# Kernel tuning notes

Hardware: AMD Instinct MI355X
Metric: run time of the kernel (lower is better)

The kernel has to match this reference:

```python
import math
import jax, jax.numpy as jnp
import numpy as np

B = 128          # batch_size (graphs)
SEQ = 128        # max_seq_len (nodes per graph)
D = 128          # input_dim
HID = 64         # enc_hidden_dim
HEADS = 4        # in_head
N = B * SEQ      # total nodes
E = 262144       # edges (avg degree 16)


def _make_pe(seq, d):
    pos = np.arange(seq, dtype=np.float32)[:, None]
    i_even = np.arange(0, d, 2, dtype=np.float32)
    pe = np.zeros((seq, d), dtype=np.float32)
    pe[:, 0::2] = np.sin(pos / 10000.0 ** (2.0 * i_even / d))
    pe[:, 1::2] = np.cos(pos / 10000.0 ** (2.0 * (i_even + 1.0) / d))
    return jnp.asarray(pe)


def setup_inputs() -> dict:
    key = jax.random.key(0)
    ks = jax.random.split(key, 10)
    s = 0.1
    return {
        "x": jax.random.normal(ks[0], (N, D), jnp.float32),
        "edge_index": jax.random.randint(ks[1], (2, E), 0, N),
        "pe": _make_pe(SEQ, D),
        "W1": jax.random.normal(ks[2], (D, HEADS * HID), jnp.float32) * s,
        "a_src1": jax.random.normal(ks[3], (HEADS, HID), jnp.float32) * s,
        "a_dst1": jax.random.normal(ks[4], (HEADS, HID), jnp.float32) * s,
        "b1": jnp.zeros((HEADS * HID,), jnp.float32),
        "W2": jax.random.normal(ks[5], (HEADS * HID, HID), jnp.float32) * s,
        "a_src2": jax.random.normal(ks[6], (1, HID), jnp.float32) * s,
        "a_dst2": jax.random.normal(ks[7], (1, HID), jnp.float32) * s,
        "b2": jnp.zeros((HID,), jnp.float32),
        "batch_size": B,
    }


def _gat_conv(x, src, dst, W, a_src, a_dst, b, heads, ch, concat, n):
    # PyG GATConv (eval mode, self-loops already appended to src/dst).
    h = (x @ W).reshape(n, heads, ch)                      # [N,H,C]
    alpha_src = jnp.einsum("nhc,hc->nh", h, a_src)         # [N,H]
    alpha_dst = jnp.einsum("nhc,hc->nh", h, a_dst)
    e = jax.nn.leaky_relu(alpha_src[src] + alpha_dst[dst], 0.2)  # [E,H]
    m = jax.ops.segment_max(e, dst, num_segments=n)        # segment softmax over dst
    ex = jnp.exp(e - m[dst])
    den = jax.ops.segment_sum(ex, dst, num_segments=n)
    alpha = ex / (den[dst] + 1e-16)                        # [E,H]
    out = jax.ops.segment_sum(h[src] * alpha[:, :, None], dst, num_segments=n)
    out = out.reshape(n, heads * ch) if concat else out.mean(axis=1)
    return out + b


def reference(x, edge_index, pe, W1, a_src1, a_dst1, b1, W2, a_src2, a_dst2, b2, batch_size):
    n = x.shape[0]
    loop = jnp.arange(n)
    src = jnp.concatenate([edge_index[0], loop])           # add self-loops (PyG default)
    dst = jnp.concatenate([edge_index[1], loop])
    # positional encoding (dropout inactive in eval)
    h = x * math.sqrt(x.shape[1]) + jnp.tile(pe, (batch_size, 1))
    h = jax.nn.elu(_gat_conv(h, src, dst, W1, a_src1, a_dst1, b1, HEADS, HID, True, n))
    out = _gat_conv(h, src, dst, W2, a_src2, a_dst2, b2, 1, HID, False, n)
    return out.reshape(batch_size, -1, out.shape[1])
```

## Files before the change

### kernel.cpp

```cpp
#include <hip/hip_runtime.h>
#include <hip/hip_bf16.h>

typedef __hip_bfloat16 bf16;
typedef __attribute__((ext_vector_type(8))) short short8v;
typedef __attribute__((ext_vector_type(4))) float f32x4;

#define N_NODES 16384
#define D_IN    128
#define HID     64
#define HEADS   4
#define F1      256
#define SEQ     128
#define SLOTS   64

__device__ __forceinline__ float wave_sum(float v) {
    #pragma unroll
    for (int o = 32; o > 0; o >>= 1) v += __shfl_xor(v, o, 64);
    return v;
}
__device__ __forceinline__ float lrelu(float v) { return v > 0.f ? v : 0.2f * v; }
__device__ __forceinline__ float bfu(unsigned short u) {
    return __uint_as_float((unsigned)u << 16);
}
__device__ __forceinline__ unsigned short f2b(float f) {
    unsigned u = __float_as_uint(f);
    return (unsigned short)((u + 0x7fffu + ((u >> 16) & 1u)) >> 16);
}

#define FMA8(u, ti)                                                  \
    do {                                                             \
        float t_ = __int_as_float(ti);                               \
        a0 += __uint_as_float((u).x << 16) * t_;                     \
        a1 += __uint_as_float((u).x & 0xffff0000u) * t_;             \
        a2 += __uint_as_float((u).y << 16) * t_;                     \
        a3 += __uint_as_float((u).y & 0xffff0000u) * t_;             \
    } while (0)

__global__ __launch_bounds__(256) void k_prep(const float* __restrict__ W1,
                                              const float* __restrict__ a_s1,
                                              const float* __restrict__ a_d1,
                                              unsigned short* __restrict__ w1hi,
                                              unsigned short* __restrict__ w1lo,
                                              float* __restrict__ gs,
                                              float* __restrict__ gd,
                                              int* __restrict__ cnt) {
    int gid = blockIdx.x * 256 + threadIdx.x;
    int j  = gid & 7;
    int l  = (gid >> 3) & 63;
    int ks = (gid >> 9) & 3;
    int n  = gid >> 11;
    int k   = ks * 32 + ((l >> 4) << 3) + j;
    int col = n * 16 + (l & 15);
    float w = W1[(size_t)k * 256 + col];
    unsigned short hi = f2b(w);
    w1hi[gid] = hi;
    w1lo[gid] = f2b(w - bfu(hi));
    if (gid < N_NODES) cnt[gid] = 0;
    if (gid < 512) {
        int kk = gid >> 2, hd = gid & 3;
        const float* wr = W1 + (size_t)kk * 256 + hd * 64;
        const float* as = a_s1 + hd * 64;
        const float* ad = a_d1 + hd * 64;
        float s = 0.f, d2 = 0.f;
        for (int c = 0; c < 64; c++) { float wv = wr[c]; s += wv * as[c]; d2 += wv * ad[c]; }
        gs[gid] = s; gd[gid] = d2;
    }
}

__global__ __launch_bounds__(256, 4) void k_gemm1m(const float* __restrict__ x,
                                                   const float* __restrict__ pe,
                                                   const unsigned short* __restrict__ w1hi,
                                                   const unsigned short* __restrict__ w1lo,
                                                   const float* __restrict__ gs,
                                                   const float* __restrict__ gd,
                                                   bf16* __restrict__ h,
                                                   float* __restrict__ as1,
                                                   float* __restrict__ ad1,
                                                   const int* __restrict__ ei, int E, int Etot,
                                                   int* __restrict__ cnt,
                                                   int* __restrict__ esrc) {
    int tid = threadIdx.x, lane = tid & 63, wv = tid >> 6;

    for (int e = blockIdx.x * 256 + tid; e < Etot; e += 262144) {
        int s, d;
        if (e < E) { s = ei[e]; d = ei[E + e]; }
        else       { s = e - E; d = s; }
        int pos = atomicAdd(&cnt[d], 1);
        if (pos < SLOTS) esrc[d * SLOTS + pos] = s;
    }

    int rowb = blockIdx.x * 16;
    int r0 = lane & 15;
    int kg = lane >> 4;
    int kb = kg * 8;

    short8v afh[4], afl[4];
    f32x4 ls = {0.f, 0.f, 0.f, 0.f};
    f32x4 ld = {0.f, 0.f, 0.f, 0.f};
    #pragma unroll
    for (int ks = 0; ks < 4; ks++) {
        const float* xp = x  + (size_t)(rowb + r0) * 128 + ks * 32 + kb;
        const float* pp = pe + (size_t)((rowb + r0) & (SEQ - 1)) * 128 + ks * 32 + kb;
        float4 xa = *(const float4*)xp;
        float4 xb = *(const float4*)(xp + 4);
        float4 pa = *(const float4*)pp;
        float4 pb = *(const float4*)(pp + 4);
        float v[8];
        v[0] = xa.x * 11.313708499f + pa.x;
        v[1] = xa.y * 11.313708499f + pa.y;
        v[2] = xa.z * 11.313708499f + pa.z;
        v[3] = xa.w * 11.313708499f + pa.w;
        v[4] = xb.x * 11.313708499f + pb.x;
        v[5] = xb.y * 11.313708499f + pb.y;
        v[6] = xb.z * 11.313708499f + pb.z;
        v[7] = xb.w * 11.313708499f + pb.w;
        short8v ah, al;
        #pragma unroll
        for (int j = 0; j < 8; j++) {
            unsigned short hi = f2b(v[j]);
            ah[j] = (short)hi;
            al[j] = (short)f2b(v[j] - bfu(hi));
        }
        afh[ks] = ah; afl[ks] = al;
        if (wv == 0) {
            #pragma unroll
            for (int j = 0; j < 8; j++) {
                int k = ks * 32 + kb + j;
                float4 g4 = *(const float4*)(gs + k * 4);
                float4 h4 = *(const float4*)(gd + k * 4);
                ls.x += v[j] * g4.x; ls.y += v[j] * g4.y;
                ls.z += v[j] * g4.z; ls.w += v[j] * g4.w;
                ld.x += v[j] * h4.x; ld.y += v[j] * h4.y;
                ld.z += v[j] * h4.z; ld.w += v[j] * h4.w;
            }
        }
    }
    if (wv == 0) {
        #pragma unroll
        for (int o = 16; o < 64; o <<= 1) {
            ls.x += __shfl_xor(ls.x, o); ls.y += __shfl_xor(ls.y, o);
            ls.z += __shfl_xor(ls.z, o); ls.w += __shfl_xor(ls.w, o);
            ld.x += __shfl_xor(ld.x, o); ld.y += __shfl_xor(ld.y, o);
            ld.z += __shfl_xor(ld.z, o); ld.w += __shfl_xor(ld.w, o);
        }
        if (lane < 16) {
            int row = rowb + lane;
            *(float4*)(as1 + row * 4) = make_float4(ls.x, ls.y, ls.z, ls.w);
            *(float4*)(ad1 + row * 4) = make_float4(ld.x, ld.y, ld.z, ld.w);
        }
    }

    const short8v* wph = (const short8v*)w1hi;
    const short8v* wpl = (const short8v*)w1lo;
    unsigned short* hu = (unsigned short*)h;
    #pragma unroll
    for (int t = 0; t < 4; t++) {
        int n = wv * 4 + t;
        f32x4 acc = {0.f, 0.f, 0.f, 0.f};
        #pragma unroll
        for (int ks = 0; ks < 4; ks++) {
            short8v bh = wph[(n * 4 + ks) * 64 + lane];
            short8v bl = wpl[(n * 4 + ks) * 64 + lane];
            acc = __builtin_amdgcn_mfma_f32_16x16x32_bf16(afh[ks], bh, acc, 0, 0, 0);
            acc = __builtin_amdgcn_mfma_f32_16x16x32_bf16(afl[ks], bh, acc, 0, 0, 0);
            acc = __builtin_amdgcn_mfma_f32_16x16x32_bf16(afh[ks], bl, acc, 0, 0, 0);
        }
        #pragma unroll
        for (int r = 0; r < 4; r++)
            hu[(size_t)(rowb + kg * 4 + r) * 256 + n * 16 + r0] = f2b(acc[r]);
    }
}

__global__ __launch_bounds__(256) void k_agg1_gemm2(
        const int* __restrict__ cnt, const int* __restrict__ esrc,
        const float* __restrict__ as1, const float* __restrict__ ad1,
        const bf16* __restrict__ h,
        const float* __restrict__ b1,
        const float* __restrict__ W2,
        const float* __restrict__ a_src2, const float* __restrict__ a_dst2,
        bf16* __restrict__ h2, float* __restrict__ as2, float* __restrict__ ad2) {
    __shared__ float hs[4][256];
    __shared__ int2  st[4][4][64];
    int tid = threadIdx.x, lane = tid & 63, wv = tid >> 6;
    int dbase = blockIdx.x * 4;
    int d = dbase + wv;
    int deg = min(cnt[d], SLOTS);
    const uint2* hb = (const uint2*)h;

    uint2 eu0, eu1, eu2, eu3;
    {
        int s = esrc[(size_t)d * SLOTS + lane] & (N_NODES - 1);
        int s0 = __shfl(s, 0), s1 = __shfl(s, 1), s2 = __shfl(s, 2), s3 = __shfl(s, 3);
        eu0 = hb[(size_t)s0 * 64 + lane];
        eu1 = hb[(size_t)s1 * 64 + lane];
        eu2 = hb[(size_t)s2 * 64 + lane];
        eu3 = hb[(size_t)s3 * 64 + lane];

        float4 av = *(const float4*)(as1 + (size_t)s * 4);
        float4 dv = *(const float4*)(ad1 + (size_t)d * 4);
        bool live = lane < deg;
        float t0 = live ? __expf(lrelu(av.x + dv.x) - 40.f) : 0.f;
        float t1 = live ? __expf(lrelu(av.y + dv.y) - 40.f) : 0.f;
        float t2 = live ? __expf(lrelu(av.z + dv.z) - 40.f) : 0.f;
        float t3 = live ? __expf(lrelu(av.w + dv.w) - 40.f) : 0.f;
        float i0 = 1.f / wave_sum(t0);
        float i1 = 1.f / wave_sum(t1);
        float i2 = 1.f / wave_sum(t2);
        float i3 = 1.f / wave_sum(t3);
        int2 p0; p0.x = s; p0.y = __float_as_int(t0 * i0); st[wv][0][lane] = p0;
        int2 p1; p1.x = s; p1.y = __float_as_int(t1 * i1); st[wv][1][lane] = p1;
        int2 p2; p2.x = s; p2.y = __float_as_int(t2 * i2); st[wv][2][lane] = p2;
        int2 p3; p3.x = s; p3.y = __float_as_int(t3 * i3); st[wv][3][lane] = p3;
    }

    {
        int hd = lane >> 4;
        const int4* stp4 = (const int4*)st[wv][hd];
        float a0 = 0.f, a1 = 0.f, a2 = 0.f, a3 = 0.f;
        int np = (deg + 1) >> 1;

        int4 P0 = stp4[0];
        int4 P1 = stp4[1];
        int4 P2 = stp4[2];
        int4 P3 = stp4[3];
        uint2 w20 = hb[(size_t)P2.x * 64 + lane];
        uint2 w21 = hb[(size_t)P2.z * 64 + lane];
        uint2 w30 = hb[(size_t)P3.x * 64 + lane];
        uint2 w31 = hb[(size_t)P3.z * 64 + lane];
        FMA8(eu0, P0.y);
        FMA8(eu1, P0.w);
        FMA8(eu2, P1.y);
        FMA8(eu3, P1.w);
        for (int q = 4; q < np; q += 2) {
            int4 N0 = stp4[q];
            int4 N1 = stp4[q + 1];
            uint2 x20 = hb[(size_t)N0.x * 64 + lane];
            uint2 x21 = hb[(size_t)N0.z * 64 + lane];
            uint2 x30 = hb[(size_t)N1.x * 64 + lane];
            uint2 x31 = hb[(size_t)N1.z * 64 + lane];
            FMA8(w20, P2.y);
            FMA8(w21, P2.w);
            FMA8(w30, P3.y);
            FMA8(w31, P3.w);
            P2 = N0; P3 = N1;
            w20 = x20; w21 = x21; w30 = x30; w31 = x31;
        }
        FMA8(w20, P2.y);
        FMA8(w21, P2.w);
        FMA8(w30, P3.y);
        FMA8(w31, P3.w);

        float4 bb = *(const float4*)(b1 + lane * 4);
        float o0 = a0 + bb.x, o1 = a1 + bb.y, o2 = a2 + bb.z, o3 = a3 + bb.w;
        o0 = o0 > 0.f ? o0 : (__expf(o0) - 1.f);
        o1 = o1 > 0.f ? o1 : (__expf(o1) - 1.f);
        o2 = o2 > 0.f ? o2 : (__expf(o2) - 1.f);
        o3 = o3 > 0.f ? o3 : (__expf(o3) - 1.f);
        *(float4*)&hs[wv][lane * 4] = make_float4(o0, o1, o2, o3);
    }
    __syncthreads();

    float* part = (float*)st;

    {
        float acc2[4] = {0, 0, 0, 0};
        const int k4base = wv * 16;
        for (int kk = 0; kk < 16; kk++) {
            int k4 = k4base + kk;
            const float* wp = W2 + (size_t)k4 * 256 + lane;
            float w0 = wp[0], w1 = wp[64], w2 = wp[128], w3 = wp[192];
            #pragma unroll
            for (int r = 0; r < 4; r++) {
                float4 u = *(const float4*)&hs[r][k4 * 4];
                acc2[r] += u.x * w0 + u.y * w1 + u.z * w2 + u.w * w3;
            }
        }
        #pragma unroll
        for (int r = 0; r < 4; r++) part[(wv * 4 + r) * 64 + lane] = acc2[r];
    }
    __syncthreads();
    {
        int r = wv;
        float a0 = part[(0 * 4 + r) * 64 + lane] + part[(1 * 4 + r) * 64 + lane]
                 + part[(2 * 4 + r) * 64 + lane] + part[(3 * 4 + r) * 64 + lane];
        float asj = a_src2[lane], adj = a_dst2[lane];
        int n0 = dbase + r;
        h2[(size_t)n0 * 64 + lane] = __float2bfloat16(a0);
        float va0 = wave_sum(a0 * asj);
        float vd0 = wave_sum(a0 * adj);
        if (lane == 0) {
            as2[n0] = va0; ad2[n0] = vd0;
        }
    }
}

__global__ __launch_bounds__(256) void k_agg2(const int* __restrict__ cnt,
                                              const int* __restrict__ esrc,
                                              const float* __restrict__ as2,
                                              const float* __restrict__ ad2,
                                              const bf16* __restrict__ h2,
                                              const float* __restrict__ b2v,
                                              float* __restrict__ out) {
    __shared__ int2 sts2[4][64];
    int tid = threadIdx.x, lane = tid & 63, wv = tid >> 6;
    int d = blockIdx.x * 4 + wv;
    int deg = min(cnt[d], SLOTS);
    int g = lane >> 4;
    int c16 = lane & 15;
    const uint2* hb2 = (const uint2*)h2;

    uint2 u0, u1;
    float tn;
    {
        int s = esrc[(size_t)d * SLOTS + lane] & (N_NODES - 1);
        int se0 = __shfl(s, g);
        int se1 = __shfl(s, 4 + g);
        u0 = hb2[(size_t)se0 * 16 + c16];
        u1 = hb2[(size_t)se1 * 16 + c16];

        float av = as2[s];
        float adw = ad2[d];
        float t = (lane < deg) ? __expf(lrelu(av + adw) - 40.f) : 0.f;
        float inv = 1.f / wave_sum(t);
        tn = t * inv;
        int2 pr; pr.x = s; pr.y = __float_as_int(tn);
        sts2[wv][lane] = pr;
    }

    float a0 = 0.f, a1 = 0.f, a2 = 0.f, a3 = 0.f;
    int nq = (deg + 3) >> 2;
    int t0i = __float_as_int(__shfl(tn, g));
    int t1i = __float_as_int(__shfl(tn, 4 + g));
    int2 P2 = sts2[wv][8 + g];
    int2 P3 = sts2[wv][12 + g];
    uint2 w2 = hb2[(size_t)P2.x * 16 + c16];
    uint2 w3 = hb2[(size_t)P3.x * 16 + c16];
    FMA8(u0, t0i);
    FMA8(u1, t1i);
    for (int q = 4; q < nq; q += 2) {
        int2 N0 = sts2[wv][4 * q + g];
        int2 N1 = sts2[wv][4 * (q + 1) + g];
        uint2 x2 = hb2[(size_t)N0.x * 16 + c16];
        uint2 x3 = hb2[(size_t)N1.x * 16 + c16];
        FMA8(w2, P2.y);
        FMA8(w3, P3.y);
        P2 = N0; P3 = N1; w2 = x2; w3 = x3;
    }
    FMA8(w2, P2.y);
    FMA8(w3, P3.y);

    #pragma unroll
    for (int o = 16; o < 64; o <<= 1) {
        a0 += __shfl_xor(a0, o);
        a1 += __shfl_xor(a1, o);
        a2 += __shfl_xor(a2, o);
        a3 += __shfl_xor(a3, o);
    }
    if (lane < 16) {
        float4 bb = *(const float4*)(b2v + c16 * 4);
        float4* dst = (float4*)(out + (size_t)d * 64 + c16 * 4);
        *dst = make_float4(a0 + bb.x, a1 + bb.y, a2 + bb.z, a3 + bb.w);
    }
}

extern "C" void kernel_launch(void* const* d_in, const int* in_sizes, int n_in,
                              void* d_out, int out_size, void* d_ws, size_t ws_size,
                              hipStream_t stream) {
    const float* x    = (const float*)d_in[0];
    const int*   ei   = (const int*)  d_in[1];
    const float* pe   = (const float*)d_in[2];
    const float* W1   = (const float*)d_in[3];
    const float* a_s1 = (const float*)d_in[4];
    const float* a_d1 = (const float*)d_in[5];
    const float* b1   = (const float*)d_in[6];
    const float* W2   = (const float*)d_in[7];
    const float* a_s2 = (const float*)d_in[8];
    const float* a_d2 = (const float*)d_in[9];
    const float* b2   = (const float*)d_in[10];

    const int E    = in_sizes[1] / 2;
    const int n    = N_NODES;
    const int Etot = E + n;

    char* p = (char*)d_ws;
    auto alloc = [&](size_t bytes) -> void* {
        void* r = (void*)p;
        p += (bytes + 255) & ~(size_t)255;
        return r;
    };
    int*   cnt     = (int*)  alloc((size_t)n * 4);
    int*   esrc    = (int*)  alloc((size_t)n * SLOTS * 4);
    bf16*  h       = (bf16*) alloc((size_t)n * F1 * 2);
    float* as1     = (float*)alloc((size_t)n * HEADS * 4);
    float* ad1     = (float*)alloc((size_t)n * HEADS * 4);
    bf16*  h2      = (bf16*) alloc((size_t)n * HID * 2);
    float* as2     = (float*)alloc((size_t)n * 4);
    float* ad2     = (float*)alloc((size_t)n * 4);
    unsigned short* w1hi = (unsigned short*)alloc((size_t)D_IN * F1 * 2);
    unsigned short* w1lo = (unsigned short*)alloc((size_t)D_IN * F1 * 2);
    float* gs      = (float*)alloc((size_t)D_IN * HEADS * 4);
    float* gd      = (float*)alloc((size_t)D_IN * HEADS * 4);

    k_prep      <<<128, 256, 0, stream>>>(W1, a_s1, a_d1, w1hi, w1lo, gs, gd, cnt);
    k_gemm1m    <<<n / 16, 256, 0, stream>>>(x, pe, w1hi, w1lo, gs, gd, h, as1, ad1,
                                             ei, E, Etot, cnt, esrc);
    k_agg1_gemm2<<<n / 4, 256, 0, stream>>>(cnt, esrc, as1, ad1, h, b1,
                                            W2, a_s2, a_d2, h2, as2, ad2);
    k_agg2      <<<n / 4, 256, 0, stream>>>(cnt, esrc, as2, ad2, h2, b2, (float*)d_out);
}
```

Baseline: 150.7 us.

## Split each destination node's layer-1 aggregation across two waves

The fused aggregation+GEMM2 kernel now assigns two waves to each destination node instead of one, each wave gathering alternate edge pairs. Partial sums are combined through shared memory before the ELU and the small W2 product, and the grid doubles to n/2 blocks. The goal is more memory-level parallelism on the latency-bound neighbor gathers. In exchange it adds an extra barrier and shared-memory reduction, and halves the reuse of each W2 load across rows in the GEMM2 stage.

```diff
diff --git a/kernel.cpp b/kernel.cpp
--- a/kernel.cpp
+++ b/kernel.cpp
@@ -104,16 +104,16 @@
         float4 xa = *(const float4*)xp;
         float4 xb = *(const float4*)(xp + 4);
         float4 pa = *(const float4*)pp;
-        float4 pb = *(const float4*)(pp + 4);
+        float4 pb4 = *(const float4*)(pp + 4);
         float v[8];
         v[0] = xa.x * 11.313708499f + pa.x;
         v[1] = xa.y * 11.313708499f + pa.y;
         v[2] = xa.z * 11.313708499f + pa.z;
         v[3] = xa.w * 11.313708499f + pa.w;
-        v[4] = xb.x * 11.313708499f + pb.x;
-        v[5] = xb.y * 11.313708499f + pb.y;
-        v[6] = xb.z * 11.313708499f + pb.z;
-        v[7] = xb.w * 11.313708499f + pb.w;
+        v[4] = xb.x * 11.313708499f + pb4.x;
+        v[5] = xb.y * 11.313708499f + pb4.y;
+        v[6] = xb.z * 11.313708499f + pb4.z;
+        v[7] = xb.w * 11.313708499f + pb4.w;
         short8v ah, al;
         #pragma unroll
         for (int j = 0; j < 8; j++) {
@@ -179,18 +179,23 @@
         const float* __restrict__ W2,
         const float* __restrict__ a_src2, const float* __restrict__ a_dst2,
         bf16* __restrict__ h2, float* __restrict__ as2, float* __restrict__ ad2) {
-    __shared__ float hs[4][256];
-    __shared__ int2  st[4][4][64];
+    __shared__ float hs[2][256];
+    __shared__ int2  st[2][4][64];
+    __shared__ float pb[2][2][256];
     int tid = threadIdx.x, lane = tid & 63, wv = tid >> 6;
-    int dbase = blockIdx.x * 4;
-    int d = dbase + wv;
+    int ni = wv >> 1, hf = wv & 1;
+    int dbase = blockIdx.x * 2;
+    int d = dbase + ni;
     int deg = min(cnt[d], SLOTS);
     const uint2* hb = (const uint2*)h;
 
     uint2 eu0, eu1, eu2, eu3;
     {
         int s = esrc[(size_t)d * SLOTS + lane] & (N_NODES - 1);
-        int s0 = __shfl(s, 0), s1 = __shfl(s, 1), s2 = __shfl(s, 2), s3 = __shfl(s, 3);
+        int s0 = __shfl(s, 2 * hf);
+        int s1 = __shfl(s, 2 * hf + 1);
+        int s2 = __shfl(s, 2 * hf + 4);
+        int s3 = __shfl(s, 2 * hf + 5);
         eu0 = hb[(size_t)s0 * 64 + lane];
         eu1 = hb[(size_t)s1 * 64 + lane];
         eu2 = hb[(size_t)s2 * 64 + lane];
@@ -207,22 +212,22 @@
         float i1 = 1.f / wave_sum(t1);
         float i2 = 1.f / wave_sum(t2);
         float i3 = 1.f / wave_sum(t3);
-        int2 p0; p0.x = s; p0.y = __float_as_int(t0 * i0); st[wv][0][lane] = p0;
-        int2 p1; p1.x = s; p1.y = __float_as_int(t1 * i1); st[wv][1][lane] = p1;
-        int2 p2; p2.x = s; p2.y = __float_as_int(t2 * i2); st[wv][2][lane] = p2;
-        int2 p3; p3.x = s; p3.y = __float_as_int(t3 * i3); st[wv][3][lane] = p3;
+        int2 p0; p0.x = s; p0.y = __float_as_int(t0 * i0); st[ni][0][lane] = p0;
+        int2 p1; p1.x = s; p1.y = __float_as_int(t1 * i1); st[ni][1][lane] = p1;
+        int2 p2; p2.x = s; p2.y = __float_as_int(t2 * i2); st[ni][2][lane] = p2;
+        int2 p3; p3.x = s; p3.y = __float_as_int(t3 * i3); st[ni][3][lane] = p3;
     }
 
     {
         int hd = lane >> 4;
-        const int4* stp4 = (const int4*)st[wv][hd];
+        const int4* stp4 = (const int4*)st[ni][hd];
         float a0 = 0.f, a1 = 0.f, a2 = 0.f, a3 = 0.f;
         int np = (deg + 1) >> 1;
 
-        int4 P0 = stp4[0];
-        int4 P1 = stp4[1];
-        int4 P2 = stp4[2];
-        int4 P3 = stp4[3];
+        int4 P0 = stp4[hf];
+        int4 P1 = stp4[hf + 2];
+        int4 P2 = stp4[hf + 4];
+        int4 P3 = stp4[hf + 6];
         uint2 w20 = hb[(size_t)P2.x * 64 + lane];
         uint2 w21 = hb[(size_t)P2.z * 64 + lane];
         uint2 w30 = hb[(size_t)P3.x * 64 + lane];
@@ -231,9 +236,9 @@
         FMA8(eu1, P0.w);
         FMA8(eu2, P1.y);
         FMA8(eu3, P1.w);
-        for (int q = 4; q < np; q += 2) {
+        for (int q = hf + 8; q < np; q += 4) {
             int4 N0 = stp4[q];
-            int4 N1 = stp4[q + 1];
+            int4 N1 = stp4[q + 2];
             uint2 x20 = hb[(size_t)N0.x * 64 + lane];
             uint2 x21 = hb[(size_t)N0.z * 64 + lane];
             uint2 x30 = hb[(size_t)N1.x * 64 + lane];
@@ -249,40 +254,47 @@
         FMA8(w21, P2.w);
         FMA8(w30, P3.y);
         FMA8(w31, P3.w);
-
+        *(float4*)&pb[ni][hf][lane * 4] = make_float4(a0, a1, a2, a3);
+    }
+    __syncthreads();
+
+    if (hf == 0) {
+        float4 pa = *(const float4*)&pb[ni][0][lane * 4];
+        float4 pq = *(const float4*)&pb[ni][1][lane * 4];
         float4 bb = *(const float4*)(b1 + lane * 4);
-        float o0 = a0 + bb.x, o1 = a1 + bb.y, o2 = a2 + bb.z, o3 = a3 + bb.w;
+        float o0 = pa.x + pq.x + bb.x, o1 = pa.y + pq.y + bb.y;
+        float o2 = pa.z + pq.z + bb.z, o3 = pa.w + pq.w + bb.w;
         o0 = o0 > 0.f ? o0 : (__expf(o0) - 1.f);
         o1 = o1 > 0.f ? o1 : (__expf(o1) - 1.f);
         o2 = o2 > 0.f ? o2 : (__expf(o2) - 1.f);
         o3 = o3 > 0.f ? o3 : (__expf(o3) - 1.f);
-        *(float4*)&hs[wv][lane * 4] = make_float4(o0, o1, o2, o3);
+        *(float4*)&hs[ni][lane * 4] = make_float4(o0, o1, o2, o3);
     }
     __syncthreads();
 
     float* part = (float*)st;
 
     {
-        float acc2[4] = {0, 0, 0, 0};
+        float acc2[2] = {0.f, 0.f};
         const int k4base = wv * 16;
         for (int kk = 0; kk < 16; kk++) {
             int k4 = k4base + kk;
             const float* wp = W2 + (size_t)k4 * 256 + lane;
             float w0 = wp[0], w1 = wp[64], w2 = wp[128], w3 = wp[192];
             #pragma unroll
-            for (int r = 0; r < 4; r++) {
+            for (int r = 0; r < 2; r++) {
                 float4 u = *(const float4*)&hs[r][k4 * 4];
                 acc2[r] += u.x * w0 + u.y * w1 + u.z * w2 + u.w * w3;
             }
         }
         #pragma unroll
-        for (int r = 0; r < 4; r++) part[(wv * 4 + r) * 64 + lane] = acc2[r];
+        for (int r = 0; r < 2; r++) part[(wv * 2 + r) * 64 + lane] = acc2[r];
     }
     __syncthreads();
-    {
+    if (wv < 2) {
         int r = wv;
-        float a0 = part[(0 * 4 + r) * 64 + lane] + part[(1 * 4 + r) * 64 + lane]
-                 + part[(2 * 4 + r) * 64 + lane] + part[(3 * 4 + r) * 64 + lane];
+        float a0 = part[(0 * 2 + r) * 64 + lane] + part[(1 * 2 + r) * 64 + lane]
+                 + part[(2 * 2 + r) * 64 + lane] + part[(3 * 2 + r) * 64 + lane];
         float asj = a_src2[lane], adj = a_dst2[lane];
         int n0 = dbase + r;
         h2[(size_t)n0 * 64 + lane] = __float2bfloat16(a0);
@@ -404,7 +416,7 @@
     k_prep      <<<128, 256, 0, stream>>>(W1, a_s1, a_d1, w1hi, w1lo, gs, gd, cnt);
     k_gemm1m    <<<n / 16, 256, 0, stream>>>(x, pe, w1hi, w1lo, gs, gd, h, as1, ad1,
                                              ei, E, Etot, cnt, esrc);
-    k_agg1_gemm2<<<n / 4, 256, 0, stream>>>(cnt, esrc, as1, ad1, h, b1,
+    k_agg1_gemm2<<<n / 2, 256, 0, stream>>>(cnt, esrc, as1, ad1, h, b1,
                                             W2, a_s2, a_d2, h2, as2, ad2);
     k_agg2      <<<n / 4, 256, 0, stream>>>(cnt, esrc, as2, ad2, h2, b2, (float*)d_out);
 }
```

New measurement: 159.3 us. 5.7% more time.
